# Kernel optimization log

Measured on AMD Instinct MI355X. Metric: run time of the kernel, lower is better.

The kernel has to match this reference:

```python
import jax, jax.numpy as jnp
import numpy as np

EMBED = 1024
HEADS = 16
HEAD_DIM = EMBED // HEADS  # 64 quantum wires


def setup_inputs() -> dict:
    key = jax.random.key(0)
    ks = jax.random.split(key, 6)
    s = 1.0 / np.sqrt(EMBED)
    return {
        "x": jax.random.normal(ks[0], (8, 4096, EMBED), dtype=jnp.float32),
        "Wk": jax.random.normal(ks[1], (EMBED, EMBED), dtype=jnp.float32) * s,
        "Wq": jax.random.normal(ks[2], (EMBED, EMBED), dtype=jnp.float32) * s,
        "Wv": jax.random.normal(ks[3], (EMBED, EMBED), dtype=jnp.float32) * s,
        "Wo": jax.random.normal(ks[4], (EMBED, EMBED), dtype=jnp.float32) * s,
        "theta": jax.random.normal(ks[5], (HEAD_DIM,), dtype=jnp.float32),
    }


def reference(x, Wk, Wq, Wv, Wo, theta):
    b, s, _ = x.shape
    # linear projections (torch Linear: y = x @ W^T), split heads -> [b,s,h,d]
    def proj(W):
        return (x @ W.T).reshape(b, s, HEADS, HEAD_DIM)
    k, q, v = proj(Wk), proj(Wq), proj(Wv)
    # QLayer: per-wire RX(x_i) then trainable RX(theta_i) on |0>, measure PauliZ
    # -> <Z_i> = cos(x_i + theta_i) exactly (product state, independent wires).
    k_q = jnp.cos(k + theta)
    q_q = jnp.cos(q + theta)
    v_q = jnp.cos(v + theta)
    # Faithful to source: matmul over last two dims of [b,s,h,d] -> attention
    # across the HEADS axis ([b,s,h,h]), not across sequence.
    scores = jnp.einsum('bsid,bsjd->bsij', q_q, k_q) / jnp.sqrt(
        jnp.asarray(HEAD_DIM, dtype=x.dtype))
    attn = jax.nn.softmax(scores, axis=-1)  # dropout = identity at inference
    out = jnp.einsum('bsij,bsjd->bsid', attn, v_q).reshape(b, s, EMBED)
    return out @ Wo.T
```

## Files before the change

### kernel.cpp

```cpp
#include <hip/hip_runtime.h>
#include <hip/hip_fp16.h>

#define NTOK 32768
#define NE   1024

typedef _Float16 half_t;
typedef _Float16 f16x8 __attribute__((ext_vector_type(8)));
typedef _Float16 f16x4 __attribute__((ext_vector_type(4)));
typedef float    f32x4 __attribute__((ext_vector_type(4)));

typedef __attribute__((address_space(1))) const unsigned int guint;
typedef __attribute__((address_space(3))) unsigned int luint;

__device__ __forceinline__ void async16(const void* g, void* l) {
    __builtin_amdgcn_global_load_lds((guint*)g, (luint*)l, 16, 0, 0);
}

__global__ __launch_bounds__(256) void cvt_f32_f16(const float* __restrict__ s,
                                                   half_t* __restrict__ d, int n) {
    int i = (blockIdx.x * 256 + threadIdx.x) * 8;
    if (i >= n) return;
    float4 a = *(const float4*)(s + i);
    float4 b = *(const float4*)(s + i + 4);
    f16x8 h = {(_Float16)a.x, (_Float16)a.y, (_Float16)a.z, (_Float16)a.w,
               (_Float16)b.x, (_Float16)b.y, (_Float16)b.z, (_Float16)b.w};
    *(f16x8*)(d + i) = h;
}


#define WAITV(N) asm volatile("s_waitcnt vmcnt(" #N ")" ::: "memory")
#define BARRIER()                              \
    do {                                       \
        asm volatile("" ::: "memory");         \
        __builtin_amdgcn_s_barrier();          \
        asm volatile("" ::: "memory");         \
    } while (0)

#define STAGE_A(dst, q, k0)                                                   \
    do {                                                                      \
        _Pragma("unroll") for (int l = 0; l < 2; ++l)                         \
            async16(Ag + (size_t)(l * 128 + (q) * 64 + rr) * K + (k0) + cc,   \
                    (char*)(dst) + l * 8192 + w * 1024);                      \
    } while (0)

#define STAGE_B(dst, r, k0)                                                   \
    do {                                                                      \
        _Pragma("unroll") for (int l = 0; l < 2; ++l)                         \
            async16(Bg + (size_t)((l * 2 + wb) * 64 + (r) * 32 + (rr & 31)) * K + \
                        (k0) + cc,                                            \
                    (char*)(dst) + l * 8192 + w * 1024);                      \
    } while (0)

#define READ_A(dstf, q)                                                       \
    do {                                                                      \
        _Pragma("unroll") for (int i = 0; i < 4; ++i)                         \
        _Pragma("unroll") for (int x = 0; x < 2; ++x)                         \
            dstf[i][x] = *(const f16x8*)&As[cur][q][(wr * 64 + i * 16 + l16) * 64 + \
                                                    (((x * 4 + quad) ^ sw) * 8)]; \
    } while (0)

#define READ_B(dstf, r)                                                       \
    do {                                                                      \
        _Pragma("unroll") for (int i2 = 0; i2 < 2; ++i2)                      \
        _Pragma("unroll") for (int x = 0; x < 2; ++x)                         \
            dstf[i2][x] = *(const f16x8*)&Bs[cur][r][(wc * 32 + i2 * 16 + l16) * 64 + \
                                                     (((x * 4 + quad) ^ sw) * 8)]; \
    } while (0)

#define MMA(af, bf, QA, RB)                                                   \
    do {                                                                      \
        __builtin_amdgcn_s_setprio(1);                                        \
        _Pragma("unroll") for (int i = 0; i < 4; ++i)                         \
        _Pragma("unroll") for (int jj = 0; jj < 2; ++jj)                      \
        _Pragma("unroll") for (int x = 0; x < 2; ++x)                         \
            acc[(QA) * 4 + i][(RB) * 2 + jj] =                                \
                __builtin_amdgcn_mfma_f32_16x16x32_f16(                       \
                    af[i][x], bf[jj][x], acc[(QA) * 4 + i][(RB) * 2 + jj], 0, 0, 0); \
        __builtin_amdgcn_s_setprio(0);                                        \
    } while (0)

template <bool QKV>
__global__ __launch_bounds__(512, 2) void gemm_bt(const half_t* __restrict__ A,
                                                  const half_t* __restrict__ Bbase,
                                                  void* __restrict__ Cout,
                                                  const float* __restrict__ theta) {
    constexpr int K  = 1024;
    constexpr int NT = 16;
    constexpr int J  = QKV ? 12 : 4;
    __shared__ alignas(16) half_t As[2][2][128 * 64];
    __shared__ alignas(16) half_t Bs[2][2][128 * 64];

    const int id    = blockIdx.x;
    const int xcd   = id & 7;
    const int slot  = id >> 3;
    const int ygrp  = slot / J;
    const int j     = slot - ygrp * J;
    const int mtile = ygrp * 8 + xcd;
    const int zsl   = QKV ? (j >> 2) : 0;
    const int xt    = QKV ? (j & 3) : j;

    const int tid  = threadIdx.x;
    const int w    = tid >> 6;
    const int lane = tid & 63;
    const int quad = lane >> 4;
    const int l16  = lane & 15;
    const int sw   = l16 & 7;
    const int wr   = w >> 2, wc = w & 3;
    const size_t m0 = (size_t)mtile * 256;
    const int    n0 = xt * 256;

    const half_t* Ag = A + m0 * K;
    const half_t* Bg = Bbase + (size_t)zsl * (size_t)(NE * NE) + (size_t)n0 * K;

    const int rr = tid >> 3;
    const int cc = ((tid & 7) ^ (rr & 7)) * 8;
    const int wb = tid >> 8;

    f32x4 acc[8][4];
#pragma unroll
    for (int i = 0; i < 8; ++i)
#pragma unroll
        for (int jj = 0; jj < 4; ++jj) acc[i][jj] = (f32x4){0.f, 0.f, 0.f, 0.f};

    STAGE_A(As[0][0], 0, 0);
    STAGE_B(Bs[0][0], 0, 0);
    STAGE_B(Bs[0][1], 1, 0);
    STAGE_A(As[0][1], 1, 0);
    STAGE_A(As[1][0], 0, 64);

    f16x8 aF[4][2], bF0[2][2], bF1[2][2];

    for (int t = 0; t < NT - 1; ++t) {
        const int cur = t & 1, nxt = cur ^ 1;
        const int kn = (t + 1) * 64;
        WAITV(6);
        BARRIER();
        STAGE_B(Bs[nxt][0], 0, kn);
        READ_A(aF, 0);
        READ_B(bF0, 0);
        MMA(aF, bF0, 0, 0);
        WAITV(6);
        BARRIER();
        STAGE_B(Bs[nxt][1], 1, kn);
        READ_B(bF1, 1);
        MMA(aF, bF1, 0, 1);
        WAITV(6);
        BARRIER();
        STAGE_A(As[nxt][1], 1, kn);
        READ_A(aF, 1);
        MMA(aF, bF1, 1, 1);
        WAITV(6);
        BARRIER();
        if (t + 2 < NT) STAGE_A(As[cur][0], 0, kn + 64);
        READ_B(bF0, 0);
        MMA(aF, bF0, 1, 0);
    }
    {
        const int cur = (NT - 1) & 1;
        WAITV(4);
        BARRIER();
        READ_A(aF, 0);
        READ_B(bF0, 0);
        MMA(aF, bF0, 0, 0);
        WAITV(2);
        BARRIER();
        READ_B(bF1, 1);
        MMA(aF, bF1, 0, 1);
        WAITV(0);
        BARRIER();
        READ_A(aF, 1);
        MMA(aF, bF1, 1, 1);
        READ_B(bF0, 0);
        MMA(aF, bF0, 1, 0);
    }

    if (QKV) {
        half_t* C = (half_t*)Cout + (size_t)zsl * ((size_t)NTOK * NE);
#pragma unroll
        for (int nt = 0; nt < 4; ++nt) {
            const int n = n0 + wc * 64 + nt * 16 + l16;
            const float th = theta[n & 63];
#pragma unroll
            for (int mt = 0; mt < 8; ++mt) {
                const size_t mb = m0 + wr * 128 + mt * 16 + quad * 4;
#pragma unroll
                for (int r = 0; r < 4; ++r)
                    C[(mb + r) * NE + n] = (half_t)__cosf(acc[mt][nt][r] + th);
            }
        }
    } else {
        float* C = (float*)Cout;
#pragma unroll
        for (int nt = 0; nt < 4; ++nt) {
            const int n = n0 + wc * 64 + nt * 16 + l16;
#pragma unroll
            for (int mt = 0; mt < 8; ++mt) {
                const size_t mb = m0 + wr * 128 + mt * 16 + quad * 4;
#pragma unroll
                for (int r = 0; r < 4; ++r) C[(mb + r) * NE + n] = acc[mt][nt][r];
            }
        }
    }
}

__global__ __launch_bounds__(256) void attn_kernel(const half_t* __restrict__ q,
                                                   const half_t* __restrict__ k,
                                                   const half_t* __restrict__ v,
                                                   half_t* __restrict__ out) {
    __shared__ half_t vT[4][64][20];
    __shared__ half_t Pl[4][16][20];
    const int tid  = threadIdx.x;
    const int w    = tid >> 6;
    const int lane = tid & 63;
    const int quad = lane >> 4;
    const int l16  = lane & 15;
    const size_t base = ((size_t)blockIdx.x * 4 + w) * 1024;

    {
        const int h = lane >> 2, d0 = (lane & 3) * 16;
        f16x8 va = *(const f16x8*)(v + base + h * 64 + d0);
        f16x8 vb = *(const f16x8*)(v + base + h * 64 + d0 + 8);
#pragma unroll
        for (int z = 0; z < 8; ++z) {
            vT[w][d0 + z][h]     = va[z];
            vT[w][d0 + 8 + z][h] = vb[z];
        }
    }

    f16x8 aq0 = *(const f16x8*)(q + base + l16 * 64 + quad * 8);
    f16x8 aq1 = *(const f16x8*)(q + base + l16 * 64 + 32 + quad * 8);
    f16x8 bk0 = *(const f16x8*)(k + base + l16 * 64 + quad * 8);
    f16x8 bk1 = *(const f16x8*)(k + base + l16 * 64 + 32 + quad * 8);
    f32x4 S = __builtin_amdgcn_mfma_f32_16x16x32_f16(aq0, bk0, (f32x4){0.f,0.f,0.f,0.f}, 0, 0, 0);
    S = __builtin_amdgcn_mfma_f32_16x16x32_f16(aq1, bk1, S, 0, 0, 0);

#pragma unroll
    for (int r = 0; r < 4; ++r) {
        float s = S[r] * 0.125f;
        float mx = s;
#pragma unroll
        for (int o = 8; o; o >>= 1) mx = fmaxf(mx, __shfl_xor(mx, o));
        float e = __expf(s - mx);
        float sum = e;
#pragma unroll
        for (int o = 8; o; o >>= 1) sum += __shfl_xor(sum, o);
        Pl[w][quad * 4 + r][l16] = (half_t)(e / sum);
    }
    __syncthreads();

    f16x4 ap = *(const f16x4*)&Pl[w][l16][quad * 4];
#pragma unroll
    for (int c = 0; c < 4; ++c) {
        f16x4 bv = *(const f16x4*)&vT[w][c * 16 + l16][quad * 4];
        f32x4 O = __builtin_amdgcn_mfma_f32_16x16x16f16(ap, bv, (f32x4){0.f,0.f,0.f,0.f}, 0, 0, 0);
#pragma unroll
        for (int r = 0; r < 4; ++r)
            out[base + (quad * 4 + r) * 64 + c * 16 + l16] = (half_t)O[r];
    }
}

extern "C" void kernel_launch(void* const* d_in, const int* in_sizes, int n_in,
                              void* d_out, int out_size, void* d_ws, size_t ws_size,
                              hipStream_t stream) {
    const float* x     = (const float*)d_in[0];
    const float* Wk    = (const float*)d_in[1];
    const float* Wq    = (const float*)d_in[2];
    const float* Wv    = (const float*)d_in[3];
    const float* Wo    = (const float*)d_in[4];
    const float* theta = (const float*)d_in[5];

    char* ws = (char*)d_ws;
    half_t* xh  = (half_t*)ws;
    half_t* wh  = (half_t*)(ws + (size_t)(64 << 20));
    half_t* qkv = (half_t*)(ws + (size_t)(72 << 20));

    cvt_f32_f16<<<NTOK * NE / 2048, 256, 0, stream>>>(x, xh, NTOK * NE);
    cvt_f32_f16<<<NE * NE / 2048, 256, 0, stream>>>(Wq, wh + 0 * NE * NE, NE * NE);
    cvt_f32_f16<<<NE * NE / 2048, 256, 0, stream>>>(Wk, wh + 1 * NE * NE, NE * NE);
    cvt_f32_f16<<<NE * NE / 2048, 256, 0, stream>>>(Wv, wh + 2 * NE * NE, NE * NE);
    cvt_f32_f16<<<NE * NE / 2048, 256, 0, stream>>>(Wo, wh + 3 * NE * NE, NE * NE);

    gemm_bt<true><<<1536, 512, 0, stream>>>(xh, wh, qkv, theta);

    attn_kernel<<<NTOK / 4, 256, 0, stream>>>(qkv, qkv + (size_t)NTOK * NE,
                                              qkv + 2 * (size_t)NTOK * NE, xh);

    gemm_bt<false><<<512, 512, 0, stream>>>(xh, wh + 3 * NE * NE, d_out, nullptr);
}
```

Baseline: 653.8 us.

## Prefetch LDS fragments ahead of MFMA and stage epilogue through LDS

Restructures the GEMM main loop so the register fragments for the next sub-tile are read from LDS while the current MFMAs run. Next-iteration A/B fragments are prefetched at the end of each iteration, and extra barriers guard buffer reuse. The epilogue now writes results into a swizzled shared-memory tile and then issues coalesced 16-byte global stores, replacing scattered 2- and 4-byte column stores. The gains are meant to come from hiding LDS latency and cutting uncoalesced global writes. The cost is more barriers per iteration, extra registers for the double fragments, and an added LDS round-trip in the epilogue.

```diff
diff --git a/kernel.cpp b/kernel.cpp
--- a/kernel.cpp
+++ b/kernel.cpp
@@ -36,6 +36,9 @@
         asm volatile("" ::: "memory");         \
     } while (0)
 
+#define ASC(b, c) (Asm + ((b) * 2 + (c)) * 8192)
+#define BSC(b, c) (Bsm + ((b) * 2 + (c)) * 8192)
+
 #define STAGE_A(dst, q, k0)                                                   \
     do {                                                                      \
         _Pragma("unroll") for (int l = 0; l < 2; ++l)                         \
@@ -51,20 +54,20 @@
                     (char*)(dst) + l * 8192 + w * 1024);                      \
     } while (0)
 
-#define READ_A(dstf, q)                                                       \
+#define READ_A(dstf, b, q)                                                    \
     do {                                                                      \
         _Pragma("unroll") for (int i = 0; i < 4; ++i)                         \
         _Pragma("unroll") for (int x = 0; x < 2; ++x)                         \
-            dstf[i][x] = *(const f16x8*)&As[cur][q][(wr * 64 + i * 16 + l16) * 64 + \
-                                                    (((x * 4 + quad) ^ sw) * 8)]; \
-    } while (0)
-
-#define READ_B(dstf, r)                                                       \
+            dstf[i][x] = *(const f16x8*)&ASC(b, q)[(wr * 64 + i * 16 + l16) * 64 + \
+                                                   (((x * 4 + quad) ^ sw) * 8)]; \
+    } while (0)
+
+#define READ_B(dstf, b, r)                                                    \
     do {                                                                      \
         _Pragma("unroll") for (int i2 = 0; i2 < 2; ++i2)                      \
         _Pragma("unroll") for (int x = 0; x < 2; ++x)                         \
-            dstf[i2][x] = *(const f16x8*)&Bs[cur][r][(wc * 32 + i2 * 16 + l16) * 64 + \
-                                                     (((x * 4 + quad) ^ sw) * 8)]; \
+            dstf[i2][x] = *(const f16x8*)&BSC(b, r)[(wc * 32 + i2 * 16 + l16) * 64 + \
+                                                    (((x * 4 + quad) ^ sw) * 8)]; \
     } while (0)
 
 #define MMA(af, bf, QA, RB)                                                   \
@@ -87,8 +90,9 @@
     constexpr int K  = 1024;
     constexpr int NT = 16;
     constexpr int J  = QKV ? 12 : 4;
-    __shared__ alignas(16) half_t As[2][2][128 * 64];
-    __shared__ alignas(16) half_t Bs[2][2][128 * 64];
+    __shared__ alignas(16) half_t smem[65536];
+    half_t* Asm = smem;
+    half_t* Bsm = smem + 32768;
 
     const int id    = blockIdx.x;
     const int xcd   = id & 7;
@@ -122,83 +126,120 @@
 #pragma unroll
         for (int jj = 0; jj < 4; ++jj) acc[i][jj] = (f32x4){0.f, 0.f, 0.f, 0.f};
 
-    STAGE_A(As[0][0], 0, 0);
-    STAGE_B(Bs[0][0], 0, 0);
-    STAGE_B(Bs[0][1], 1, 0);
-    STAGE_A(As[0][1], 1, 0);
-    STAGE_A(As[1][0], 0, 64);
-
-    f16x8 aF[4][2], bF0[2][2], bF1[2][2];
+    STAGE_A(ASC(0, 0), 0, 0);
+    STAGE_B(BSC(0, 0), 0, 0);
+    STAGE_B(BSC(0, 1), 1, 0);
+    STAGE_A(ASC(0, 1), 1, 0);
+    STAGE_A(ASC(1, 0), 0, 64);
+    WAITV(6);
+    BARRIER();
+
+    f16x8 aF0[4][2], aF1[4][2], bF0[2][2], bF1[2][2];
+    READ_A(aF0, 0, 0);
+    READ_B(bF0, 0, 0);
 
     for (int t = 0; t < NT - 1; ++t) {
         const int cur = t & 1, nxt = cur ^ 1;
         const int kn = (t + 1) * 64;
-        WAITV(6);
-        BARRIER();
-        STAGE_B(Bs[nxt][0], 0, kn);
-        READ_A(aF, 0);
-        READ_B(bF0, 0);
-        MMA(aF, bF0, 0, 0);
-        WAITV(6);
-        BARRIER();
-        STAGE_B(Bs[nxt][1], 1, kn);
-        READ_B(bF1, 1);
-        MMA(aF, bF1, 0, 1);
-        WAITV(6);
-        BARRIER();
-        STAGE_A(As[nxt][1], 1, kn);
-        READ_A(aF, 1);
-        MMA(aF, bF1, 1, 1);
-        WAITV(6);
-        BARRIER();
-        if (t + 2 < NT) STAGE_A(As[cur][0], 0, kn + 64);
-        READ_B(bF0, 0);
-        MMA(aF, bF0, 1, 0);
+        WAITV(4);
+        BARRIER();
+        STAGE_B(BSC(nxt, 0), 0, kn);
+        MMA(aF0, bF0, 0, 0);
+        READ_B(bF1, cur, 1);
+        BARRIER();
+        WAITV(4);
+        BARRIER();
+        STAGE_B(BSC(nxt, 1), 1, kn);
+        MMA(aF0, bF1, 0, 1);
+        READ_A(aF1, cur, 1);
+        BARRIER();
+        WAITV(4);
+        BARRIER();
+        STAGE_A(ASC(nxt, 1), 1, kn);
+        MMA(aF1, bF1, 1, 1);
+        BARRIER();
+        WAITV(4);
+        BARRIER();
+        if (t + 2 < NT) STAGE_A(ASC(cur, 0), 0, kn + 64);
+        MMA(aF1, bF0, 1, 0);
+        READ_A(aF0, nxt, 0);
+        READ_B(bF0, nxt, 0);
+        BARRIER();
     }
     {
-        const int cur = (NT - 1) & 1;
-        WAITV(4);
-        BARRIER();
-        READ_A(aF, 0);
-        READ_B(bF0, 0);
-        MMA(aF, bF0, 0, 0);
         WAITV(2);
         BARRIER();
-        READ_B(bF1, 1);
-        MMA(aF, bF1, 0, 1);
+        MMA(aF0, bF0, 0, 0);
+        READ_B(bF1, 1, 1);
+        BARRIER();
         WAITV(0);
         BARRIER();
-        READ_A(aF, 1);
-        MMA(aF, bF1, 1, 1);
-        READ_B(bF0, 0);
-        MMA(aF, bF0, 1, 0);
-    }
+        MMA(aF0, bF1, 0, 1);
+        READ_A(aF1, 1, 1);
+        BARRIER();
+        MMA(aF1, bF1, 1, 1);
+        MMA(aF1, bF0, 1, 0);
+    }
+    __syncthreads();
 
     if (QKV) {
-        half_t* C = (half_t*)Cout + (size_t)zsl * ((size_t)NTOK * NE);
+        half_t* Cl = smem;
 #pragma unroll
         for (int nt = 0; nt < 4; ++nt) {
-            const int n = n0 + wc * 64 + nt * 16 + l16;
-            const float th = theta[n & 63];
+            const int col = wc * 64 + nt * 16 + l16;
+            const float th = theta[col & 63];
 #pragma unroll
             for (int mt = 0; mt < 8; ++mt) {
-                const size_t mb = m0 + wr * 128 + mt * 16 + quad * 4;
-#pragma unroll
-                for (int r = 0; r < 4; ++r)
-                    C[(mb + r) * NE + n] = (half_t)__cosf(acc[mt][nt][r] + th);
+                const int rowb = wr * 128 + mt * 16 + quad * 4;
+#pragma unroll
+                for (int r = 0; r < 4; ++r) {
+                    const int row = rowb + r;
+                    Cl[row * 256 + (col ^ (((row >> 2) & 3) << 4))] =
+                        (half_t)__cosf(acc[mt][nt][r] + th);
+                }
             }
         }
+        __syncthreads();
+        half_t* Cg = (half_t*)Cout + (size_t)zsl * ((size_t)NTOK * NE);
+#pragma unroll
+        for (int it = 0; it < 16; ++it) {
+            const int row = it * 16 + (tid >> 5);
+            const int seg = tid & 31;
+            f16x8 vv = *(const f16x8*)&Cl[row * 256 +
+                                          ((seg * 8) ^ (((row >> 2) & 3) << 4))];
+            *(f16x8*)&Cg[(m0 + row) * NE + n0 + seg * 8] = vv;
+        }
     } else {
-        float* C = (float*)Cout;
-#pragma unroll
-        for (int nt = 0; nt < 4; ++nt) {
-            const int n = n0 + wc * 64 + nt * 16 + l16;
-#pragma unroll
-            for (int mt = 0; mt < 8; ++mt) {
-                const size_t mb = m0 + wr * 128 + mt * 16 + quad * 4;
-#pragma unroll
-                for (int r = 0; r < 4; ++r) C[(mb + r) * NE + n] = acc[mt][nt][r];
+        float* ClF = (float*)smem;
+        float* Cg  = (float*)Cout;
+#pragma unroll
+        for (int s = 0; s < 2; ++s) {
+            if (wr == s) {
+#pragma unroll
+                for (int nt = 0; nt < 4; ++nt) {
+                    const int col = wc * 64 + nt * 16 + l16;
+#pragma unroll
+                    for (int mt = 0; mt < 8; ++mt) {
+                        const int rowb = mt * 16 + quad * 4;
+#pragma unroll
+                        for (int r = 0; r < 4; ++r) {
+                            const int row = rowb + r;
+                            ClF[row * 256 + (col ^ (((row >> 2) & 1) << 4))] =
+                                acc[mt][nt][r];
+                        }
+                    }
+                }
             }
+            __syncthreads();
+#pragma unroll
+            for (int it = 0; it < 16; ++it) {
+                const int row = it * 8 + (tid >> 6);
+                const int seg = tid & 63;
+                f32x4 vv = *(const f32x4*)&ClF[row * 256 +
+                                               ((seg * 4) ^ (((row >> 2) & 1) << 4))];
+                *(f32x4*)&Cg[(m0 + s * 128 + row) * NE + n0 + seg * 4] = vv;
+            }
+            __syncthreads();
         }
     }
 }
```

New measurement: 558.8 us. -14.5%, faster.
